# Performance work log

Hardware: AMD Instinct MI355X
Metric: run time of the kernel (lower is better)

Reference implementation:

```python
import jax, jax.numpy as jnp
import numpy as np

N_NODES = 50000
N_HEDGES = 5000
NNZ = 800000
IN_C = 128
D1 = 256
D2 = D1 // 4  # 64


def setup_inputs() -> dict:
    key = jax.random.key(0)
    ks = jax.random.split(key, 7)
    x = jax.random.normal(ks[0], (N_NODES, IN_C), dtype=jnp.float32)
    node_idx = jax.random.randint(ks[1], (NNZ,), 0, N_NODES, dtype=jnp.int32)
    hedge_idx = jax.random.randint(ks[2], (NNZ,), 0, N_HEDGES, dtype=jnp.int32)
    edge = jnp.stack([node_idx, hedge_idx], axis=0)  # [2, nnz]
    W1 = jax.random.normal(ks[3], (IN_C, D1), dtype=jnp.float32) / np.float32(np.sqrt(IN_C))
    b1 = jnp.zeros((D1,), dtype=jnp.float32)
    W2 = jax.random.normal(ks[4], (D1, D2), dtype=jnp.float32) / np.float32(np.sqrt(D1))
    b2 = jnp.zeros((D2,), dtype=jnp.float32)
    return {"x": x, "edge": edge, "W1": W1, "b1": b1, "W2": W2, "b2": b2}


def _hconv(x, W, b, node_idx, hedge_idx):
    # HypergraphConv (no attention, unit hyperedge weights):
    # out = D^{-1} H B^{-1} H^T (X W) + b
    xw = x @ W  # [N, F]
    ones = jnp.ones((node_idx.shape[0],), dtype=xw.dtype)
    deg = jax.ops.segment_sum(ones, node_idx, num_segments=N_NODES)      # D_i
    Dinv = jnp.where(deg > 0, 1.0 / deg, 0.0)
    cnt = jax.ops.segment_sum(ones, hedge_idx, num_segments=N_HEDGES)    # B_e
    Binv = jnp.where(cnt > 0, 1.0 / cnt, 0.0)
    # node -> hyperedge aggregation (gather + segment_sum), normalized by B^{-1}
    e = jax.ops.segment_sum(xw[node_idx], hedge_idx, num_segments=N_HEDGES) * Binv[:, None]
    # hyperedge -> node aggregation, normalized by D^{-1}
    out = jax.ops.segment_sum(e[hedge_idx], node_idx, num_segments=N_NODES) * Dinv[:, None]
    return out + b


def reference(x, edge, W1, b1, W2, b2):
    node_idx, hedge_idx = edge[0], edge[1]
    h = jax.nn.relu(_hconv(x, W1, b1, node_idx, hedge_idx))
    out = jax.nn.relu(_hconv(h, W2, b2, node_idx, hedge_idx))
    return out
```

## Files before the change

kernel.cpp:

```cpp
#include <hip/hip_runtime.h>

#define N_NODES 50000
#define N_HEDGES 5000
#define NNZ 800000
#define IN_C 128
#define D1 256
#define D2 64
#define SN 64
#define SH 256

#define HBK 20
#define NHB 250
#define HCAP 4096
#define NBK 100
#define NNB 500
#define NCAP 2048
#define BKT_BLOCKS ((NNZ + 2047) / 2048)

typedef unsigned int u32;
typedef unsigned short u16;
typedef __attribute__((ext_vector_type(8))) short short8;
typedef __attribute__((ext_vector_type(4))) float f32x4;

__device__ __forceinline__ float bf_lo(u32 u) { return __uint_as_float(u << 16); }
__device__ __forceinline__ float bf_hi(u32 u) { return __uint_as_float(u & 0xffff0000u); }
__device__ __forceinline__ u32 rne16(float f) {
    u32 u = __float_as_uint(f);
    return (u + 0x7fffu + ((u >> 16) & 1u)) >> 16;
}
__device__ __forceinline__ u32 pack2(float a, float b) {
    return rne16(a) | (rne16(b) << 16);
}
__device__ __forceinline__ void acc8(float* a, uint4 v) {
    a[0] += bf_lo(v.x); a[1] += bf_hi(v.x);
    a[2] += bf_lo(v.y); a[3] += bf_hi(v.y);
    a[4] += bf_lo(v.z); a[5] += bf_hi(v.z);
    a[6] += bf_lo(v.w); a[7] += bf_hi(v.w);
}

__global__ void cast_bucket(const float4* __restrict__ x, uint2* __restrict__ xb,
                            const float* __restrict__ W1, u16* __restrict__ w1hi,
                            u16* __restrict__ w1lo,
                            const float* __restrict__ W2, u16* __restrict__ w2hi,
                            u16* __restrict__ w2lo,
                            const int* __restrict__ nidx, const int* __restrict__ hidx,
                            int* __restrict__ gcur_h, int* __restrict__ gcur_n,
                            u32* __restrict__ pairs_h, u32* __restrict__ pairs_n) {
    __shared__ int hist_h[NHB], hist_n[NNB];
    __shared__ int base_h[NHB], base_n[NNB];
    int tid = threadIdx.x;
    int i = blockIdx.x * 256 + tid;
    float4 v = x[i];
    uint2 o;
    o.x = pack2(v.x, v.y);
    o.y = pack2(v.z, v.w);
    xb[i] = o;
    if (i < 32768) {
        int j = i & 7;
        int l = (i >> 3) & 63;
        int ct = (i >> 9) & 15;
        int kc = i >> 13;
        int k = kc * 32 + (l >> 4) * 8 + j;
        int n = ct * 16 + (l & 15);
        float w = W1[k * D1 + n];
        u32 h = rne16(w);
        w1hi[i] = (u16)h;
        w1lo[i] = (u16)rne16(w - bf_lo(h));
    } else if (i < 32768 + 16384) {
        int t = i - 32768;
        int j = t & 7;
        int l = (t >> 3) & 63;
        int nt = (t >> 9) & 3;
        int kc = t >> 11;
        int k = kc * 32 + (l >> 4) * 8 + j;
        int n = nt * 16 + (l & 15);
        float w = W2[k * D2 + n];
        u32 h = rne16(w);
        w2hi[t] = (u16)h;
        w2lo[t] = (u16)rne16(w - bf_lo(h));
    }
    if (blockIdx.x >= BKT_BLOCKS) return;
    for (int t = tid; t < NHB; t += 256) hist_h[t] = 0;
    for (int t = tid; t < NNB; t += 256) hist_n[t] = 0;
    __syncthreads();
    int e0 = blockIdx.x * 2048 + tid * 8;
    int ns[8], hs_[8];
#pragma unroll
    for (int k = 0; k < 8; k++) {
        int e = e0 + k;
        if (e < NNZ) {
            ns[k] = nidx[e];
            hs_[k] = hidx[e];
            atomicAdd(&hist_h[hs_[k] / HBK], 1);
            atomicAdd(&hist_n[ns[k] / NBK], 1);
        } else {
            ns[k] = -1;
        }
    }
    __syncthreads();
    if (tid < NHB) base_h[tid] = atomicAdd(&gcur_h[tid], hist_h[tid]);
    for (int t = tid; t < NNB; t += 256) base_n[t] = atomicAdd(&gcur_n[t], hist_n[t]);
    __syncthreads();
    for (int t = tid; t < NHB; t += 256) hist_h[t] = 0;
    for (int t = tid; t < NNB; t += 256) hist_n[t] = 0;
    __syncthreads();
#pragma unroll
    for (int k = 0; k < 8; k++) {
        if (ns[k] >= 0) {
            int n = ns[k], h = hs_[k];
            int bh = h / HBK, bn = n / NBK;
            int s1 = base_h[bh] + atomicAdd(&hist_h[bh], 1);
            if (s1 < HCAP) pairs_h[bh * HCAP + s1] = ((u32)h << 16) | (u32)n;
            int s2 = base_n[bn] + atomicAdd(&hist_n[bn], 1);
            if (s2 < NCAP) pairs_n[bn * NCAP + s2] = ((u32)n << 16) | (u32)h;
        }
    }
}

__global__ void build_adj(const u32* __restrict__ pairs_h, const int* __restrict__ gcur_h,
                          u16* __restrict__ adj_h, int* __restrict__ cur_h,
                          const u32* __restrict__ pairs_n, const int* __restrict__ gcur_n,
                          u16* __restrict__ adj_n, int* __restrict__ cur_n) {
    __shared__ u16 rows[NBK * SN];
    __shared__ int cnt[NBK];
    int tid = threadIdx.x;
    if (blockIdx.x < NHB) {
        int b = blockIdx.x;
        if (tid < HBK) cnt[tid] = 0;
        __syncthreads();
        int np = gcur_h[b];
        if (np > HCAP) np = HCAP;
        for (int t = tid; t < np; t += 256) {
            u32 p = pairs_h[b * HCAP + t];
            int hl = (int)(p >> 16) - b * HBK;
            int s = atomicAdd(&cnt[hl], 1);
            if (s < SH) rows[hl * SH + s] = (u16)(p & 0xffff);
        }
        __syncthreads();
        u32* dst = (u32*)(adj_h + b * HBK * SH);
        const u32* srcl = (const u32*)rows;
        for (int t = tid; t < HBK * SH / 2; t += 256) dst[t] = srcl[t];
        if (tid < HBK) cur_h[b * HBK + tid] = cnt[tid];
    } else {
        int b = blockIdx.x - NHB;
        if (tid < NBK) cnt[tid] = 0;
        __syncthreads();
        int np = gcur_n[b];
        if (np > NCAP) np = NCAP;
        for (int t = tid; t < np; t += 256) {
            u32 p = pairs_n[b * NCAP + t];
            int nl = (int)(p >> 16) - b * NBK;
            int s = atomicAdd(&cnt[nl], 1);
            if (s < SN) rows[nl * SN + s] = (u16)(p & 0xffff);
        }
        __syncthreads();
        u32* dst = (u32*)(adj_n + b * NBK * SN);
        const u32* srcl = (const u32*)rows;
        for (int t = tid; t < NBK * SN / 2; t += 256) dst[t] = srcl[t];
        if (tid < NBK) cur_n[b * NBK + tid] = cnt[tid];
    }
}

template <int F, int S, int SPLIT>
__global__ void gather_split(const uint4* __restrict__ src, const int* __restrict__ cur,
                             const u16* __restrict__ adj, uint4* __restrict__ dst,
                             int nrows) {
    constexpr int L = F / 8;
    constexpr int TR = L * SPLIT;
    constexpr int RB = 256 / TR;
    constexpr int CHUNK = S / SPLIT;
    int tid = threadIdx.x;
    int rl = tid / TR;
    int seg = (tid % TR) / L;
    int c = tid % L;
    int row = blockIdx.x * RB + rl;
    bool valid = row < nrows;
    int len = valid ? cur[row] : 0;
    int lenc = (len < S) ? len : S;
    int js = seg * CHUNK;
    int je = (lenc < js + CHUNK) ? lenc : (js + CHUNK);
    float a0[8] = {0,0,0,0,0,0,0,0}, a1[8] = {0,0,0,0,0,0,0,0};
    float a2[8] = {0,0,0,0,0,0,0,0}, a3[8] = {0,0,0,0,0,0,0,0};
    if (valid) {
        const u16* arow = adj + row * S;
        int j = js;
        for (; j + 7 < je; j += 8) {
            uint4 aa = *(const uint4*)(arow + j);
            int i0 = aa.x & 0xffff, i1 = aa.x >> 16;
            int i2 = aa.y & 0xffff, i3 = aa.y >> 16;
            int i4 = aa.z & 0xffff, i5 = aa.z >> 16;
            int i6 = aa.w & 0xffff, i7 = aa.w >> 16;
            uint4 v0 = src[i0 * L + c];
            uint4 v1 = src[i1 * L + c];
            uint4 v2 = src[i2 * L + c];
            uint4 v3 = src[i3 * L + c];
            uint4 v4 = src[i4 * L + c];
            uint4 v5 = src[i5 * L + c];
            uint4 v6 = src[i6 * L + c];
            uint4 v7 = src[i7 * L + c];
            acc8(a0, v0); acc8(a1, v1); acc8(a2, v2); acc8(a3, v3);
            acc8(a0, v4); acc8(a1, v5); acc8(a2, v6); acc8(a3, v7);
        }
        for (; j < je; j++) {
            uint4 v = src[(int)arow[j] * L + c];
            acc8(a0, v);
        }
    }
    __shared__ float partf[256][8];
#pragma unroll
    for (int t = 0; t < 8; t++) partf[tid][t] = ((a0[t] + a1[t]) + (a2[t] + a3[t]));
    __syncthreads();
    if (seg == 0 && valid) {
        float r[8];
#pragma unroll
        for (int t = 0; t < 8; t++) r[t] = partf[tid][t];
#pragma unroll
        for (int s2 = 1; s2 < SPLIT; s2++) {
#pragma unroll
            for (int t = 0; t < 8; t++) r[t] += partf[tid + s2 * L][t];
        }
        float inv = (len > 0) ? 1.f / (float)len : 0.f;
        uint4 o;
        o.x = pack2(r[0] * inv, r[1] * inv);
        o.y = pack2(r[2] * inv, r[3] * inv);
        o.z = pack2(r[4] * inv, r[5] * inv);
        o.w = pack2(r[6] * inv, r[7] * inv);
        dst[row * L + c] = o;
    }
}

template <int F, int S, bool BIAS_RELU, bool DST_BF16>
__global__ void gatherb(const uint4* __restrict__ src, const int* __restrict__ cur,
                        const u16* __restrict__ adj, const float4* __restrict__ bias,
                        void* __restrict__ dst, int nrows) {
    constexpr int L = F / 8;
    int gid = blockIdx.x * 256 + threadIdx.x;
    int row = gid / L;
    if (row >= nrows) return;
    int c = gid - row * L;
    int len = cur[row];
    int lenc = (len < S) ? len : S;
    int s = row * S, e = s + lenc;
    float a0[8] = {0,0,0,0,0,0,0,0}, a1[8] = {0,0,0,0,0,0,0,0};
    float a2[8] = {0,0,0,0,0,0,0,0}, a3[8] = {0,0,0,0,0,0,0,0};
    int j = s;
    for (; j + 7 < e; j += 8) {
        uint4 aa = *(const uint4*)(adj + j);
        int i0 = aa.x & 0xffff, i1 = aa.x >> 16;
        int i2 = aa.y & 0xffff, i3 = aa.y >> 16;
        int i4 = aa.z & 0xffff, i5 = aa.z >> 16;
        int i6 = aa.w & 0xffff, i7 = aa.w >> 16;
        uint4 v0 = src[i0 * L + c];
        uint4 v1 = src[i1 * L + c];
        uint4 v2 = src[i2 * L + c];
        uint4 v3 = src[i3 * L + c];
        uint4 v4 = src[i4 * L + c];
        uint4 v5 = src[i5 * L + c];
        uint4 v6 = src[i6 * L + c];
        uint4 v7 = src[i7 * L + c];
        acc8(a0, v0); acc8(a1, v1); acc8(a2, v2); acc8(a3, v3);
        acc8(a0, v4); acc8(a1, v5); acc8(a2, v6); acc8(a3, v7);
    }
    for (; j < e; j++) {
        uint4 v = src[(int)adj[j] * L + c];
        acc8(a0, v);
    }
    float inv = (len > 0) ? 1.f / (float)len : 0.f;
    float r[8];
#pragma unroll
    for (int t = 0; t < 8; t++) r[t] = ((a0[t] + a1[t]) + (a2[t] + a3[t])) * inv;
    if (BIAS_RELU) {
        float4 b0 = bias[c * 2], b1v = bias[c * 2 + 1];
        r[0] = fmaxf(r[0] + b0.x, 0.f); r[1] = fmaxf(r[1] + b0.y, 0.f);
        r[2] = fmaxf(r[2] + b0.z, 0.f); r[3] = fmaxf(r[3] + b0.w, 0.f);
        r[4] = fmaxf(r[4] + b1v.x, 0.f); r[5] = fmaxf(r[5] + b1v.y, 0.f);
        r[6] = fmaxf(r[6] + b1v.z, 0.f); r[7] = fmaxf(r[7] + b1v.w, 0.f);
    }
    if (DST_BF16) {
        uint4 o;
        o.x = pack2(r[0], r[1]);
        o.y = pack2(r[2], r[3]);
        o.z = pack2(r[4], r[5]);
        o.w = pack2(r[6], r[7]);
        ((uint4*)dst)[row * L + c] = o;
    } else {
        float4* d = (float4*)dst;
        d[row * (F / 4) + c * 2]     = make_float4(r[0], r[1], r[2], r[3]);
        d[row * (F / 4) + c * 2 + 1] = make_float4(r[4], r[5], r[6], r[7]);
    }
}

#define HSTRIDE 264
__global__ __launch_bounds__(256, 3)
void mlp64(const u16* __restrict__ sb,
           const short8* __restrict__ w1hi, const short8* __restrict__ w1lo,
           const float* __restrict__ b1,
           const short8* __restrict__ w2hi, const short8* __restrict__ w2lo,
           u16* __restrict__ hw) {
    __shared__ u16 hs[64 * HSTRIDE];
    int tid = threadIdx.x;
    int node0 = blockIdx.x * 64;
    int wave = tid >> 6;
    int lane = tid & 63;
    int m = lane & 15;
    int q = lane >> 4;
    f32x4 acc[4][4];
#pragma unroll
    for (int i = 0; i < 4; i++) {
        float bc = b1[(wave * 4 + i) * 16 + m];
#pragma unroll
        for (int mt = 0; mt < 4; mt++)
            acc[i][mt] = (f32x4){bc, bc, bc, bc};
    }
#pragma unroll
    for (int kc = 0; kc < 4; kc++) {
        short8 am[4];
#pragma unroll
        for (int mt = 0; mt < 4; mt++)
            am[mt] = *(const short8*)&sb[(node0 + mt * 16 + m) * IN_C + kc * 32 + q * 8];
        short8 w[4];
#pragma unroll
        for (int i = 0; i < 4; i++)
            w[i] = w1hi[(kc * 16 + wave * 4 + i) * 64 + lane];
#pragma unroll
        for (int i = 0; i < 4; i++)
#pragma unroll
            for (int mt = 0; mt < 4; mt++)
                acc[i][mt] = __builtin_amdgcn_mfma_f32_16x16x32_bf16(am[mt], w[i], acc[i][mt], 0, 0, 0);
#pragma unroll
        for (int i = 0; i < 4; i++)
            w[i] = w1lo[(kc * 16 + wave * 4 + i) * 64 + lane];
#pragma unroll
        for (int i = 0; i < 4; i++)
#pragma unroll
            for (int mt = 0; mt < 4; mt++)
                acc[i][mt] = __builtin_amdgcn_mfma_f32_16x16x32_bf16(am[mt], w[i], acc[i][mt], 0, 0, 0);
    }
#pragma unroll
    for (int i = 0; i < 4; i++) {
        int col = (wave * 4 + i) * 16 + m;
#pragma unroll
        for (int mt = 0; mt < 4; mt++)
#pragma unroll
            for (int r = 0; r < 4; r++) {
                float h = fmaxf(acc[i][mt][r], 0.f);
                hs[(mt * 16 + q * 4 + r) * HSTRIDE + col] = (u16)rne16(h);
            }
    }
    __syncthreads();
    f32x4 acc2[4];
#pragma unroll
    for (int mt = 0; mt < 4; mt++) acc2[mt] = (f32x4){0.f, 0.f, 0.f, 0.f};
#pragma unroll
    for (int kc = 0; kc < 8; kc++) {
        short8 ah[4];
#pragma unroll
        for (int mt = 0; mt < 4; mt++)
            ah[mt] = *(const short8*)&hs[(mt * 16 + m) * HSTRIDE + kc * 32 + q * 8];
        short8 whi = w2hi[(kc * 4 + wave) * 64 + lane];
#pragma unroll
        for (int mt = 0; mt < 4; mt++)
            acc2[mt] = __builtin_amdgcn_mfma_f32_16x16x32_bf16(ah[mt], whi, acc2[mt], 0, 0, 0);
        short8 wlo = w2lo[(kc * 4 + wave) * 64 + lane];
#pragma unroll
        for (int mt = 0; mt < 4; mt++)
            acc2[mt] = __builtin_amdgcn_mfma_f32_16x16x32_bf16(ah[mt], wlo, acc2[mt], 0, 0, 0);
    }
#pragma unroll
    for (int mt = 0; mt < 4; mt++)
#pragma unroll
        for (int r = 0; r < 4; r++) {
            int row = node0 + mt * 16 + q * 4 + r;
            if (row < N_NODES)
                hw[row * D2 + wave * 16 + m] = (u16)rne16(acc2[mt][r]);
        }
}

extern "C" void kernel_launch(void* const* d_in, const int* in_sizes, int n_in,
                              void* d_out, int out_size, void* d_ws, size_t ws_size,
                              hipStream_t stream) {
    const float* x  = (const float*)d_in[0];
    const int* edge = (const int*)d_in[1];
    const int* nidx = edge;
    const int* hidx = edge + NNZ;
    const float* W1 = (const float*)d_in[2];
    const float* b1 = (const float*)d_in[3];
    const float* W2 = (const float*)d_in[4];
    const float* b2 = (const float*)d_in[5];
    float* out = (float*)d_out;

    u16* xb     = (u16*)d_ws;
    u16* aggxb  = xb + N_NODES * IN_C;
    u16* hwb    = aggxb + N_HEDGES * IN_C;
    u16* e2b    = hwb + N_NODES * D2;
    u16* w1hi   = e2b + N_HEDGES * D2;
    u16* w1lo   = w1hi + 32768;
    u16* w2hi   = w1lo + 32768;
    u16* w2lo   = w2hi + 16384;
    u16* adj_n  = w2lo + 16384;
    u16* adj_h  = adj_n + N_NODES * SN;
    u32* pairs_h = (u32*)(adj_h + N_HEDGES * SH);
    u32* pairs_n = pairs_h + NHB * HCAP;
    int* cur_n  = (int*)(pairs_n + NNB * NCAP);
    int* cur_h  = cur_n + N_NODES;
    int* gcur_h = cur_h + N_HEDGES;
    int* gcur_n = gcur_h + 256;
    u16* sb     = (u16*)(gcur_n + 512);

    hipMemsetAsync(gcur_h, 0, (256 + 512) * sizeof(int), stream);

    cast_bucket<<<N_NODES * IN_C / 4 / 256, 256, 0, stream>>>(
        (const float4*)x, (uint2*)xb, W1, w1hi, w1lo, W2, w2hi, w2lo,
        nidx, hidx, gcur_h, gcur_n, pairs_h, pairs_n);

    build_adj<<<NHB + NNB, 256, 0, stream>>>(pairs_h, gcur_h, adj_h, cur_h,
                                             pairs_n, gcur_n, adj_n, cur_n);

    gather_split<IN_C, SH, 4><<<(N_HEDGES + 3) / 4, 256, 0, stream>>>(
        (const uint4*)xb, cur_h, adj_h, (uint4*)aggxb, N_HEDGES);

    gatherb<IN_C, SN, false, true><<<(N_NODES * (IN_C / 8) + 255) / 256, 256, 0, stream>>>(
        (const uint4*)aggxb, cur_n, adj_n, (const float4*)b1, (void*)sb, N_NODES);

    mlp64<<<(N_NODES + 63) / 64, 256, 0, stream>>>(
        sb, (const short8*)w1hi, (const short8*)w1lo, b1,
        (const short8*)w2hi, (const short8*)w2lo, hwb);

    gather_split<D2, SH, 8><<<(N_HEDGES + 3) / 4, 256, 0, stream>>>(
        (const uint4*)hwb, cur_h, adj_h, (uint4*)e2b, N_HEDGES);
    gatherb<D2, SN, true, false><<<(N_NODES * (D2 / 8) + 255) / 256, 256, 0, stream>>>(
        (const uint4*)e2b, cur_n, adj_n, (const float4*)b2, out, N_NODES);
}
```

Baseline: 222.1 us.

## Pad adjacency rows with zero dummy rows to drop gather tail loops

Adds a zeroed dummy row after each source feature buffer and pre-fills the adjacency row slots with that dummy index, so each gather loop rounds its length up to a multiple of eight and drops the scalar remainder loop. The index vector for the next iteration is prefetched inside a shared gather core, and the gather kernels get launch bounds hinting two blocks per SIMD. This trades a few extra loads of a cached zero row and extra shared-memory fill work in build_adj for branch-free, fully unrolled gathers.

```diff
diff --git a/kernel.cpp b/kernel.cpp
--- a/kernel.cpp
+++ b/kernel.cpp
@@ -9,6 +9,9 @@
 #define SN 64
 #define SH 256
 
+#define DUMN 50000
+#define DUMH 5000
+
 #define HBK 20
 #define NHB 250
 #define HCAP 4096
@@ -45,7 +48,9 @@
                             u16* __restrict__ w2lo,
                             const int* __restrict__ nidx, const int* __restrict__ hidx,
                             int* __restrict__ gcur_h, int* __restrict__ gcur_n,
-                            u32* __restrict__ pairs_h, u32* __restrict__ pairs_n) {
+                            u32* __restrict__ pairs_h, u32* __restrict__ pairs_n,
+                            uint4* __restrict__ xbz, uint4* __restrict__ aggz,
+                            uint4* __restrict__ hwz, uint4* __restrict__ e2z) {
     __shared__ int hist_h[NHB], hist_n[NNB];
     __shared__ int base_h[NHB], base_n[NNB];
     int tid = threadIdx.x;
@@ -79,6 +84,13 @@
         w2hi[t] = (u16)h;
         w2lo[t] = (u16)rne16(w - bf_lo(h));
     }
+    if (blockIdx.x == gridDim.x - 1) {
+        uint4 z = make_uint4(0u, 0u, 0u, 0u);
+        if (tid < 16) xbz[tid] = z;
+        else if (tid < 32) aggz[tid - 16] = z;
+        else if (tid < 40) hwz[tid - 32] = z;
+        else if (tid < 48) e2z[tid - 40] = z;
+    }
     if (blockIdx.x >= BKT_BLOCKS) return;
     for (int t = tid; t < NHB; t += 256) hist_h[t] = 0;
     for (int t = tid; t < NNB; t += 256) hist_n[t] = 0;
@@ -127,6 +139,10 @@
     if (blockIdx.x < NHB) {
         int b = blockIdx.x;
         if (tid < HBK) cnt[tid] = 0;
+        {
+            u32* rw = (u32*)rows;
+            for (int t = tid; t < HBK * SH / 2; t += 256) rw[t] = (DUMN << 16) | DUMN;
+        }
         __syncthreads();
         int np = gcur_h[b];
         if (np > HCAP) np = HCAP;
@@ -144,6 +160,10 @@
     } else {
         int b = blockIdx.x - NHB;
         if (tid < NBK) cnt[tid] = 0;
+        {
+            u32* rw = (u32*)rows;
+            for (int t = tid; t < NBK * SN / 2; t += 256) rw[t] = (DUMH << 16) | DUMH;
+        }
         __syncthreads();
         int np = gcur_n[b];
         if (np > NCAP) np = NCAP;
@@ -161,91 +181,16 @@
     }
 }
 
-template <int F, int S, int SPLIT>
-__global__ void gather_split(const uint4* __restrict__ src, const int* __restrict__ cur,
-                             const u16* __restrict__ adj, uint4* __restrict__ dst,
-                             int nrows) {
-    constexpr int L = F / 8;
-    constexpr int TR = L * SPLIT;
-    constexpr int RB = 256 / TR;
-    constexpr int CHUNK = S / SPLIT;
-    int tid = threadIdx.x;
-    int rl = tid / TR;
-    int seg = (tid % TR) / L;
-    int c = tid % L;
-    int row = blockIdx.x * RB + rl;
-    bool valid = row < nrows;
-    int len = valid ? cur[row] : 0;
-    int lenc = (len < S) ? len : S;
-    int js = seg * CHUNK;
-    int je = (lenc < js + CHUNK) ? lenc : (js + CHUNK);
-    float a0[8] = {0,0,0,0,0,0,0,0}, a1[8] = {0,0,0,0,0,0,0,0};
-    float a2[8] = {0,0,0,0,0,0,0,0}, a3[8] = {0,0,0,0,0,0,0,0};
-    if (valid) {
-        const u16* arow = adj + row * S;
-        int j = js;
-        for (; j + 7 < je; j += 8) {
-            uint4 aa = *(const uint4*)(arow + j);
-            int i0 = aa.x & 0xffff, i1 = aa.x >> 16;
-            int i2 = aa.y & 0xffff, i3 = aa.y >> 16;
-            int i4 = aa.z & 0xffff, i5 = aa.z >> 16;
-            int i6 = aa.w & 0xffff, i7 = aa.w >> 16;
-            uint4 v0 = src[i0 * L + c];
-            uint4 v1 = src[i1 * L + c];
-            uint4 v2 = src[i2 * L + c];
-            uint4 v3 = src[i3 * L + c];
-            uint4 v4 = src[i4 * L + c];
-            uint4 v5 = src[i5 * L + c];
-            uint4 v6 = src[i6 * L + c];
-            uint4 v7 = src[i7 * L + c];
-            acc8(a0, v0); acc8(a1, v1); acc8(a2, v2); acc8(a3, v3);
-            acc8(a0, v4); acc8(a1, v5); acc8(a2, v6); acc8(a3, v7);
-        }
-        for (; j < je; j++) {
-            uint4 v = src[(int)arow[j] * L + c];
-            acc8(a0, v);
-        }
-    }
-    __shared__ float partf[256][8];
-#pragma unroll
-    for (int t = 0; t < 8; t++) partf[tid][t] = ((a0[t] + a1[t]) + (a2[t] + a3[t]));
-    __syncthreads();
-    if (seg == 0 && valid) {
-        float r[8];
-#pragma unroll
-        for (int t = 0; t < 8; t++) r[t] = partf[tid][t];
-#pragma unroll
-        for (int s2 = 1; s2 < SPLIT; s2++) {
-#pragma unroll
-            for (int t = 0; t < 8; t++) r[t] += partf[tid + s2 * L][t];
-        }
-        float inv = (len > 0) ? 1.f / (float)len : 0.f;
-        uint4 o;
-        o.x = pack2(r[0] * inv, r[1] * inv);
-        o.y = pack2(r[2] * inv, r[3] * inv);
-        o.z = pack2(r[4] * inv, r[5] * inv);
-        o.w = pack2(r[6] * inv, r[7] * inv);
-        dst[row * L + c] = o;
-    }
-}
-
-template <int F, int S, bool BIAS_RELU, bool DST_BF16>
-__global__ void gatherb(const uint4* __restrict__ src, const int* __restrict__ cur,
-                        const u16* __restrict__ adj, const float4* __restrict__ bias,
-                        void* __restrict__ dst, int nrows) {
-    constexpr int L = F / 8;
-    int gid = blockIdx.x * 256 + threadIdx.x;
-    int row = gid / L;
-    if (row >= nrows) return;
-    int c = gid - row * L;
-    int len = cur[row];
-    int lenc = (len < S) ? len : S;
-    int s = row * S, e = s + lenc;
-    float a0[8] = {0,0,0,0,0,0,0,0}, a1[8] = {0,0,0,0,0,0,0,0};
-    float a2[8] = {0,0,0,0,0,0,0,0}, a3[8] = {0,0,0,0,0,0,0,0};
-    int j = s;
-    for (; j + 7 < e; j += 8) {
-        uint4 aa = *(const uint4*)(adj + j);
+template <int L>
+__device__ __forceinline__ void gcore(const uint4* __restrict__ src,
+                                      const u16* __restrict__ arow,
+                                      int js, int je, int c,
+                                      float* a0, float* a1, float* a2, float* a3) {
+    if (js >= je) return;
+    uint4 aa = *(const uint4*)(arow + js);
+    for (int j = js; j < je; j += 8) {
+        uint4 nx = aa;
+        if (j + 8 < je) nx = *(const uint4*)(arow + j + 8);
         int i0 = aa.x & 0xffff, i1 = aa.x >> 16;
         int i2 = aa.y & 0xffff, i3 = aa.y >> 16;
         int i4 = aa.z & 0xffff, i5 = aa.z >> 16;
@@ -260,11 +205,73 @@
         uint4 v7 = src[i7 * L + c];
         acc8(a0, v0); acc8(a1, v1); acc8(a2, v2); acc8(a3, v3);
         acc8(a0, v4); acc8(a1, v5); acc8(a2, v6); acc8(a3, v7);
-    }
-    for (; j < e; j++) {
-        uint4 v = src[(int)adj[j] * L + c];
-        acc8(a0, v);
-    }
+        aa = nx;
+    }
+}
+
+template <int F, int S, int SPLIT>
+__global__ __launch_bounds__(256, 2)
+void gather_split(const uint4* __restrict__ src, const int* __restrict__ cur,
+                  const u16* __restrict__ adj, uint4* __restrict__ dst,
+                  int nrows) {
+    constexpr int L = F / 8;
+    constexpr int TR = L * SPLIT;
+    constexpr int RB = 256 / TR;
+    constexpr int CHUNK = S / SPLIT;
+    int tid = threadIdx.x;
+    int rl = tid / TR;
+    int seg = (tid % TR) / L;
+    int c = tid % L;
+    int row = blockIdx.x * RB + rl;
+    bool valid = row < nrows;
+    int len = valid ? cur[row] : 0;
+    int lenc = (len < S) ? len : S;
+    int lenp = (lenc + 7) & ~7;
+    int js = seg * CHUNK;
+    int je = (lenp < js + CHUNK) ? lenp : (js + CHUNK);
+    float a0[8] = {0,0,0,0,0,0,0,0}, a1[8] = {0,0,0,0,0,0,0,0};
+    float a2[8] = {0,0,0,0,0,0,0,0}, a3[8] = {0,0,0,0,0,0,0,0};
+    if (valid)
+        gcore<L>(src, adj + row * S, js, je, c, a0, a1, a2, a3);
+    __shared__ float partf[256][8];
+#pragma unroll
+    for (int t = 0; t < 8; t++) partf[tid][t] = ((a0[t] + a1[t]) + (a2[t] + a3[t]));
+    __syncthreads();
+    if (seg == 0 && valid) {
+        float r[8];
+#pragma unroll
+        for (int t = 0; t < 8; t++) r[t] = partf[tid][t];
+#pragma unroll
+        for (int s2 = 1; s2 < SPLIT; s2++) {
+#pragma unroll
+            for (int t = 0; t < 8; t++) r[t] += partf[tid + s2 * L][t];
+        }
+        float inv = (len > 0) ? 1.f / (float)len : 0.f;
+        uint4 o;
+        o.x = pack2(r[0] * inv, r[1] * inv);
+        o.y = pack2(r[2] * inv, r[3] * inv);
+        o.z = pack2(r[4] * inv, r[5] * inv);
+        o.w = pack2(r[6] * inv, r[7] * inv);
+        dst[row * L + c] = o;
+    }
+}
+
+template <int F, int S, bool BIAS_RELU, bool DST_BF16>
+__global__ __launch_bounds__(256, 2)
+void gatherb(const uint4* __restrict__ src, const int* __restrict__ cur,
+             const u16* __restrict__ adj, const float4* __restrict__ bias,
+             void* __restrict__ dst, int nrows) {
+    constexpr int L = F / 8;
+    int gid = blockIdx.x * 256 + threadIdx.x;
+    int row = gid / L;
+    if (row >= nrows) return;
+    int c = gid - row * L;
+    int len = cur[row];
+    int lenc = (len < S) ? len : S;
+    int lenp = (lenc + 7) & ~7;
+    float a0[8] = {0,0,0,0,0,0,0,0}, a1[8] = {0,0,0,0,0,0,0,0};
+    float a2[8] = {0,0,0,0,0,0,0,0}, a3[8] = {0,0,0,0,0,0,0,0};
+    gcore<L>(src, adj + row * S, 0, lenp, c, a0, a1, a2, a3);
     float inv = (len > 0) ? 1.f / (float)len : 0.f;
     float r[8];
 #pragma unroll
@@ -390,10 +397,10 @@
     float* out = (float*)d_out;
 
     u16* xb     = (u16*)d_ws;
-    u16* aggxb  = xb + N_NODES * IN_C;
-    u16* hwb    = aggxb + N_HEDGES * IN_C;
-    u16* e2b    = hwb + N_NODES * D2;
-    u16* w1hi   = e2b + N_HEDGES * D2;
+    u16* aggxb  = xb + (N_NODES + 1) * IN_C;
+    u16* hwb    = aggxb + (N_HEDGES + 1) * IN_C;
+    u16* e2b    = hwb + (N_NODES + 1) * D2;
+    u16* w1hi   = e2b + (N_HEDGES + 1) * D2;
     u16* w1lo   = w1hi + 32768;
     u16* w2hi   = w1lo + 32768;
     u16* w2lo   = w2hi + 16384;
@@ -411,7 +418,9 @@
 
     cast_bucket<<<N_NODES * IN_C / 4 / 256, 256, 0, stream>>>(
         (const float4*)x, (uint2*)xb, W1, w1hi, w1lo, W2, w2hi, w2lo,
-        nidx, hidx, gcur_h, gcur_n, pairs_h, pairs_n);
+        nidx, hidx, gcur_h, gcur_n, pairs_h, pairs_n,
+        (uint4*)(xb + DUMN * IN_C), (uint4*)(aggxb + DUMH * IN_C),
+        (uint4*)(hwb + DUMN * D2), (uint4*)(e2b + DUMH * D2));
 
     build_adj<<<NHB + NNB, 256, 0, stream>>>(pairs_h, gcur_h, adj_h, cur_h,
                                              pairs_n, gcur_n, adj_n, cur_n);
```

After: 201.7 us (median of 2 runs). 1.1x faster.
